# Performance work log

Hardware: AMD Instinct MI355X
Metric: run time of the kernel (lower is better)

## Reference

```python
import jax, jax.numpy as jnp
import numpy as np

D = 128  # feature = hidden = output dim (residuals force equality)


def setup_inputs() -> dict:
    key = jax.random.key(0)
    kx, k1, k2, kr = jax.random.split(key, 4)
    B, N = 8, 2048
    x = jax.random.normal(kx, (B, N, D), dtype=jnp.float32)
    w1 = jax.random.normal(k1, (D, D), dtype=jnp.float32)
    w2 = jax.random.normal(k2, (D, D), dtype=jnp.float32)
    wr = jax.random.normal(kr, (D, D), dtype=jnp.float32)
    return {"x": x, "w1": w1, "w2": w2, "wr": wr}


def reference(x, w1, w2, wr):
    # bilinear scores: [B, N, N]
    R = jnp.einsum('bnf,fg,bmg->bnm', x, wr, x)
    R = jax.nn.softmax(R, axis=2)
    # layer 1: relu(R @ x @ w1 + x)
    x = jax.nn.relu(jnp.einsum('bnm,bmf->bnf', R, x) @ w1 + x)
    # layer 2: relu(R @ x @ w2 + x)
    x = jax.nn.relu(jnp.einsum('bnm,bmf->bnf', R, x) @ w2 + x)
    return x[:, 0, :]
```

## Files before the change

kernel.cpp:

```cpp
#include <hip/hip_runtime.h>
#include <stdint.h>

typedef float  f32x4 __attribute__((ext_vector_type(4)));
typedef short  s16x8 __attribute__((ext_vector_type(8)));
typedef unsigned int u32;
typedef u32    u32x2 __attribute__((ext_vector_type(2)));
typedef u32    u32x4 __attribute__((ext_vector_type(4)));
typedef unsigned short u16;

#define MFMA16(a,b,c) __builtin_amdgcn_mfma_f32_16x16x32_bf16((a),(b),(c),0,0,0)

__device__ __forceinline__ u16 f2bf(float f){
  u32 u = __float_as_uint(f);
  return (u16)((u + 0x7fffu + ((u >> 16) & 1u)) >> 16);
}
__device__ __forceinline__ float bf2f(u16 h){ return __uint_as_float(((u32)h) << 16); }
__device__ __forceinline__ u32 pack2bf(float a, float b){ return (u32)f2bf(a) | ((u32)f2bf(b) << 16); }
__device__ __forceinline__ u32 packtrunc(float a, float b){
  return (__float_as_uint(a) >> 16) | (__float_as_uint(b) & 0xffff0000u);
}
__device__ __forceinline__ f32x4 f4zero(){ f32x4 z; z[0]=0.f; z[1]=0.f; z[2]=0.f; z[3]=0.f; return z; }
__device__ __forceinline__ s16x8 mk8(u32 a, u32 b, u32 c, u32 d){
  u32x4 w; w[0]=a; w[1]=b; w[2]=c; w[3]=d;
  return __builtin_bit_cast(s16x8, w);
}

__device__ __forceinline__ void async16(const void* g, void* l){
  __builtin_amdgcn_global_load_lds(
      (const __attribute__((address_space(1))) unsigned int*)g,
      (__attribute__((address_space(3))) unsigned int*)l, 16, 0, 0);
}

__global__ __launch_bounds__(256) void k_prep(
    const float* __restrict__ x, const float* __restrict__ wr, const float* __restrict__ w1,
    u16* __restrict__ xh, u16* __restrict__ xl, u16* __restrict__ Xt,
    u16* __restrict__ w1t, u16* __restrict__ yh, u16* __restrict__ yl)
{
  __shared__ __align__(16) char smem[65536];
  const int tid = threadIdx.x, bid = blockIdx.x;

  if (bid < 1024){
    float (*xs)[132] = (float(*)[132])smem;
    const long base = (long)bid * 2048;
#pragma unroll
    for (int k = 0; k < 8; k++){
      int idx = tid + k*256;
      float v = x[base + idx];
      xs[idx>>7][idx&127] = v;
      u16 h = f2bf(v);
      xh[base+idx] = h;
      xl[base+idx] = f2bf(v - bf2f(h));
    }
    __syncthreads();
    const int b  = bid >> 7;
    const int n0 = (bid & 127) * 16;
    const int nn = tid & 15, d0 = tid >> 4;
#pragma unroll
    for (int d = 0; d < 8; d++){
      int dd = d0 + d*16;
      Xt[(long)b*262144 + (long)dd*2048 + n0 + nn] = f2bf(xs[nn][dd]);
    }
  } else if (bid < 1032){
    const int base = (bid - 1024) * 2048;
#pragma unroll
    for (int k = 0; k < 8; k++){
      int idx = base + k*256 + tid;
      int c = idx >> 7, f = idx & 127;
      w1t[idx] = f2bf(w1[f*128 + c]);
    }
  } else {
    u16* sbh = (u16*)smem;
    u16* sbl = sbh + 16384;
    {
      const int c = tid & 127, f0 = (tid >> 7) * 64;
      const int key = (c & 7) << 4;
#pragma unroll
      for (int fi = 0; fi < 64; fi += 2){
        int f = f0 + fi;
        float v0 = wr[f*128 + c], v1 = wr[(f+1)*128 + c];
        u16 h0 = f2bf(v0), h1 = f2bf(v1);
        u32 hw = (u32)h0 | ((u32)h1 << 16);
        u32 lw = (u32)f2bf(v0 - bf2f(h0)) | ((u32)f2bf(v1 - bf2f(h1)) << 16);
        int byte = c*256 + ((((2*f) & ~15) ^ key) + ((2*f) & 15));
        *(u32*)((char*)sbh + byte) = hw;
        *(u32*)((char*)sbl + byte) = lw;
      }
    }
    __syncthreads();
    const int w = tid >> 6, lane = tid & 63, lr = lane & 15, g = lane >> 4;
    const long rowbase = (long)(bid - 1032)*128 + w*32;
    s16x8 ah[2][4], al[2][4];
#pragma unroll
    for (int rh = 0; rh < 2; rh++)
#pragma unroll
      for (int kc = 0; kc < 4; kc++){
        long r = rowbase + rh*16 + lr;
        const float4* px = (const float4*)(x + r*128 + kc*32 + g*8);
        float4 a = px[0], bV = px[1];
        u32 hh0, hh1, hh2, hh3, ll0, ll1, ll2, ll3;
        { u16 p=f2bf(a.x), q=f2bf(a.y); hh0=(u32)p|((u32)q<<16);
          ll0=(u32)f2bf(a.x-bf2f(p))|((u32)f2bf(a.y-bf2f(q))<<16); }
        { u16 p=f2bf(a.z), q=f2bf(a.w); hh1=(u32)p|((u32)q<<16);
          ll1=(u32)f2bf(a.z-bf2f(p))|((u32)f2bf(a.w-bf2f(q))<<16); }
        { u16 p=f2bf(bV.x), q=f2bf(bV.y); hh2=(u32)p|((u32)q<<16);
          ll2=(u32)f2bf(bV.x-bf2f(p))|((u32)f2bf(bV.y-bf2f(q))<<16); }
        { u16 p=f2bf(bV.z), q=f2bf(bV.w); hh3=(u32)p|((u32)q<<16);
          ll3=(u32)f2bf(bV.z-bf2f(p))|((u32)f2bf(bV.w-bf2f(q))<<16); }
        ah[rh][kc] = mk8(hh0,hh1,hh2,hh3);
        al[rh][kc] = mk8(ll0,ll1,ll2,ll3);
      }
    f32x4 acc[2][8];
#pragma unroll
    for (int rh = 0; rh < 2; rh++)
#pragma unroll
      for (int cg = 0; cg < 8; cg++) acc[rh][cg] = f4zero();
    const int swz = (lr & 7) << 4;
#pragma unroll
    for (int cg = 0; cg < 8; cg++){
      const int rowt = (cg*16 + lr) * 256;
#pragma unroll
      for (int kc = 0; kc < 4; kc++){
        int boff = rowt + ((kc*64 + g*16) ^ swz);
        s16x8 bh = *(const s16x8*)((const char*)sbh + boff);
        s16x8 bl = *(const s16x8*)((const char*)sbl + boff);
#pragma unroll
        for (int rh = 0; rh < 2; rh++){
          acc[rh][cg] = MFMA16(ah[rh][kc], bh, acc[rh][cg]);
          acc[rh][cg] = MFMA16(al[rh][kc], bh, acc[rh][cg]);
          acc[rh][cg] = MFMA16(ah[rh][kc], bl, acc[rh][cg]);
        }
      }
    }
#pragma unroll
    for (int rh = 0; rh < 2; rh++)
#pragma unroll
      for (int cg = 0; cg < 8; cg++)
#pragma unroll
        for (int r = 0; r < 4; r++){
          long q = rowbase + rh*16 + 4*g + r;
          int  c = cg*16 + lr;
          float v = acc[rh][cg][r] * 1.4426950408889634f;
          u16 h = f2bf(v);
          yh[q*128 + c] = h;
          yl[q*128 + c] = f2bf(v - bf2f(h));
        }
  }
}

__global__ __launch_bounds__(512) void k_flash(
    const u16* __restrict__ xh, const u16* __restrict__ xl, const u16* __restrict__ Xt,
    const u16* __restrict__ yh, const u16* __restrict__ yl,
    u16* __restrict__ Opart, float* __restrict__ mpart, float* __restrict__ lpart,
    float* __restrict__ S0, int KS, int kslog)
{
  __shared__ __align__(16) char lds[49152];
  const int tid = threadIdx.x, bid = blockIdx.x;
  const int b     = bid & 7;
  const int inner = bid >> 3;
  const int s     = inner & (KS - 1);
  const int qbl   = inner >> kslog;
  const int qb    = b*16 + qbl;
  const int nspan = 2048 >> kslog;
  const int kv0   = s * nspan;
  const int ntiles = nspan >> 5;
  const int w = tid >> 6, lane = tid & 63, lr = lane & 15, g = lane >> 4;
  const long qrow = (long)qb*128 + w*16;

  const int soff = w*1024 + lane*16;
  const int sswo = soff ^ (((soff >> 8) & 7) << 4);
  const int trow = soff >> 6;
  const int tsrc = trow*4096 + ((soff & 63) ^ ((trow & 3) << 4));
  const int bS0 = lr*256 + (( 0 + g*16) ^ ((lr & 7) << 4));
  const int bS1 = lr*256 + (( 64 + g*16) ^ ((lr & 7) << 4));
  const int bS2 = lr*256 + ((128 + g*16) ^ ((lr & 7) << 4));
  const int bS3 = lr*256 + ((192 + g*16) ^ ((lr & 7) << 4));
  const int bPV = lr*64 + ((g*16) ^ ((lr & 3) << 4));

  s16x8 byh[4], byl[4];
#pragma unroll
  for (int kc = 0; kc < 4; kc++){
    long r = qrow + lr;
    byh[kc] = *(const s16x8*)(yh + r*128 + kc*32 + g*8);
    byl[kc] = *(const s16x8*)(yl + r*128 + kc*32 + g*8);
  }

  f32x4 o[8];
#pragma unroll
  for (int dg = 0; dg < 8; dg++) o[dg] = f4zero();
  float mrun = -1e30f, lrun = 0.f;

  const char* gxh  = (const char*)xh + ((long)b*2048 + kv0)*256;
  const char* gxl  = (const char*)xl + ((long)b*2048 + kv0)*256;
  const char* gxtb = (const char*)(Xt + (long)b*262144 + kv0);

  auto stage = [&](int bufi, int t){
    char* dst = lds + bufi*8192 + w*1024;
    async16(gxh  + (long)t*8192 + sswo, dst);
    async16(gxl  + (long)t*8192 + sswo, dst + 16384);
    async16(gxtb + (long)t*64   + tsrc, dst + 32768);
  };

  stage(0, 0);
  __syncthreads();

  for (int t = 0; t < ntiles; t++){
    const int cur = t & 1;
    const char* pb = lds + cur*8192;
    const char* a0 = pb + bS0;
    const char* a1 = pb + bS1;
    const char* a2 = pb + bS2;
    const char* a3 = pb + bS3;

    f32x4 sacc[2];
    sacc[0] = f4zero(); sacc[1] = f4zero();
    __builtin_amdgcn_s_setprio(1);
#pragma unroll
    for (int ch = 0; ch < 2; ch++){
      const int co = ch*4096;
      s16x8 fh, fl;
      fh = *(const s16x8*)(a0 + co); fl = *(const s16x8*)(a0 + 16384 + co);
      sacc[ch] = MFMA16(fh, byh[0], sacc[ch]);
      sacc[ch] = MFMA16(fl, byh[0], sacc[ch]);
      sacc[ch] = MFMA16(fh, byl[0], sacc[ch]);
      fh = *(const s16x8*)(a1 + co); fl = *(const s16x8*)(a1 + 16384 + co);
      sacc[ch] = MFMA16(fh, byh[1], sacc[ch]);
      sacc[ch] = MFMA16(fl, byh[1], sacc[ch]);
      sacc[ch] = MFMA16(fh, byl[1], sacc[ch]);
      fh = *(const s16x8*)(a2 + co); fl = *(const s16x8*)(a2 + 16384 + co);
      sacc[ch] = MFMA16(fh, byh[2], sacc[ch]);
      sacc[ch] = MFMA16(fl, byh[2], sacc[ch]);
      sacc[ch] = MFMA16(fh, byl[2], sacc[ch]);
      fh = *(const s16x8*)(a3 + co); fl = *(const s16x8*)(a3 + 16384 + co);
      sacc[ch] = MFMA16(fh, byh[3], sacc[ch]);
      sacc[ch] = MFMA16(fl, byh[3], sacc[ch]);
      sacc[ch] = MFMA16(fh, byl[3], sacc[ch]);
    }
    __builtin_amdgcn_s_setprio(0);

    if (t + 1 < ntiles) stage(cur ^ 1, t + 1);

    if (qbl == 0 && w == 0 && lr == 0){
      float* s0p = S0 + b*2048 + kv0 + t*32 + 4*g;
#pragma unroll
      for (int ch = 0; ch < 2; ch++)
#pragma unroll
        for (int r = 0; r < 4; r++)
          s0p[ch*16 + r] = sacc[ch][r];
    }

    float cm = fmaxf(fmaxf(fmaxf(sacc[0][0], sacc[0][1]),
                           fmaxf(sacc[0][2], sacc[0][3])),
                     fmaxf(fmaxf(sacc[1][0], sacc[1][1]),
                           fmaxf(sacc[1][2], sacc[1][3])));
    cm = fmaxf(cm, __shfl_xor(cm, 16, 64));
    cm = fmaxf(cm, __shfl_xor(cm, 32, 64));
    if (__any(cm > mrun + 8.f)){
      float mn = fmaxf(mrun, cm);
      float sc = exp2f(mrun - mn);
#pragma unroll
      for (int dg = 0; dg < 8; dg++)
#pragma unroll
        for (int r = 0; r < 4; r++) o[dg][r] *= sc;
      lrun *= sc;
      mrun = mn;
    }
    float p[2][4];
#pragma unroll
    for (int ch = 0; ch < 2; ch++)
#pragma unroll
      for (int r = 0; r < 4; r++) p[ch][r] = exp2f(sacc[ch][r] - mrun);
    float ls = ((p[0][0] + p[0][1]) + (p[0][2] + p[0][3]))
             + ((p[1][0] + p[1][1]) + (p[1][2] + p[1][3]));
    ls += __shfl_xor(ls, 16, 64);
    ls += __shfl_xor(ls, 32, 64);
    lrun += ls;
    s16x8 bpq;
    {
      u32 pw00 = packtrunc(p[0][0], p[0][1]);
      u32 pw01 = packtrunc(p[0][2], p[0][3]);
      u32 pw10 = packtrunc(p[1][0], p[1][1]);
      u32 pw11 = packtrunc(p[1][2], p[1][3]);
      int sA = ((g & 1) << 5) + lr;
      int sB = sA + 16;
      u32 a0s = (u32)__shfl((int)pw00, sA, 64);
      u32 a1s = (u32)__shfl((int)pw01, sA, 64);
      u32 a2s = (u32)__shfl((int)pw10, sA, 64);
      u32 a3s = (u32)__shfl((int)pw11, sA, 64);
      u32 b0s = (u32)__shfl((int)pw00, sB, 64);
      u32 b1s = (u32)__shfl((int)pw01, sB, 64);
      u32 b2s = (u32)__shfl((int)pw10, sB, 64);
      u32 b3s = (u32)__shfl((int)pw11, sB, 64);
      bool hi = (g >= 2);
      bpq = mk8(hi ? a2s : a0s, hi ? a3s : a1s, hi ? b2s : b0s, hi ? b3s : b1s);
    }

    const char* ap = pb + 32768 + bPV;
    __builtin_amdgcn_s_setprio(1);
#pragma unroll
    for (int half = 0; half < 2; half++){
      s16x8 ax[4];
#pragma unroll
      for (int i = 0; i < 4; i++)
        ax[i] = *(const s16x8*)(ap + (half*4 + i)*1024);
#pragma unroll
      for (int i = 0; i < 4; i++)
        o[half*4 + i] = MFMA16(ax[i], bpq, o[half*4 + i]);
    }
    __builtin_amdgcn_s_setprio(0);
    __syncthreads();
  }

  {
    int lq = w*16 + lr;
    long bi = (long)(qbl*8 + b)*128 + lq;
    u16* op = Opart + bi*(long)(128 << kslog) + s*128;
#pragma unroll
    for (int dg = 0; dg < 8; dg++){
      u32x2 pw;
      pw[0] = pack2bf(o[dg][0], o[dg][1]);
      pw[1] = pack2bf(o[dg][2], o[dg][3]);
      *(u32x2*)(op + dg*16 + 4*g) = pw;
    }
    if (g == 0){
      mpart[bi*KS + s] = mrun;
      lpart[bi*KS + s] = lrun;
    }
  }
}

__global__ __launch_bounds__(256) void k_mergeL1(
    const u16* __restrict__ Opart, const float* __restrict__ mpart, const float* __restrict__ lpart,
    const u16* __restrict__ w1t, const float* __restrict__ x,
    const float* __restrict__ S0,
    float* __restrict__ A2p, float* __restrict__ Lj, float* __restrict__ x1r0,
    int KS)
{
  __shared__ u16 sb[16384];
  __shared__ u16 sa[4096];
  __shared__ float eS[32];
  __shared__ float redw[4][64];
  const int tid = threadIdx.x, bid = blockIdx.x;
  const int bb   = bid >> 6;
  const int qbl  = (bid >> 2) & 15;
  const int rb   = (bid & 3) * 32;
  const long R0  = (long)bid*32;
#pragma unroll
  for (int k = 0; k < 8; k++){
    int off = (tid + k*256)*16;
    int row = off >> 8;
    *(s16x8*)((char*)sb + (off ^ ((row & 7) << 4))) = *(const s16x8*)((const char*)w1t + off);
  }
  if (tid < 32){
    const float* mp0 = mpart + (long)(bb*128)*KS;
    float M = -1e30f;
    for (int s = 0; s < KS; s++) M = fmaxf(M, mp0[s]);
    eS[tid] = exp2f(S0[bb*2048 + (bid & 63)*32 + tid] - M);
  }
#pragma unroll
  for (int k = 0; k < 2; k++){
    int gidx = tid + k*256;
    int lrow = gidx >> 4, gcol = gidx & 15;
    long bi = (long)(qbl*8 + bb)*128 + rb + lrow;
    const float* mp = mpart + bi*KS;
    const float* lp = lpart + bi*KS;
    float m = -1e30f;
    for (int s = 0; s < KS; s++) m = fmaxf(m, mp[s]);
    float ls = 0.f;
    float a0=0.f,a1=0.f,a2=0.f,a3=0.f,a4=0.f,a5=0.f,a6=0.f,a7=0.f;
    const u16* ob = Opart + bi*(long)(KS*128) + gcol*8;
    for (int s = 0; s < KS; s++){
      float wgt = exp2f(mp[s] - m);
      ls += lp[s] * wgt;
      u32x4 v = *(const u32x4*)(ob + s*128);
      a0 += bf2f((u16)(v[0] & 0xffff)) * wgt;  a1 += bf2f((u16)(v[0] >> 16)) * wgt;
      a2 += bf2f((u16)(v[1] & 0xffff)) * wgt;  a3 += bf2f((u16)(v[1] >> 16)) * wgt;
      a4 += bf2f((u16)(v[2] & 0xffff)) * wgt;  a5 += bf2f((u16)(v[2] >> 16)) * wgt;
      a6 += bf2f((u16)(v[3] & 0xffff)) * wgt;  a7 += bf2f((u16)(v[3] >> 16)) * wgt;
    }
    float inv = 1.f / ls;
    u32x4 pw;
    pw[0] = pack2bf(a0*inv, a1*inv); pw[1] = pack2bf(a2*inv, a3*inv);
    pw[2] = pack2bf(a4*inv, a5*inv); pw[3] = pack2bf(a6*inv, a7*inv);
    int off = lrow*256 + gcol*16;
    *(u32x4*)((char*)sa + (off ^ ((lrow & 7) << 4))) = pw;
  }
  __syncthreads();
  const int w = tid >> 6, lane = tid & 63, lr = lane & 15, g = lane >> 4;
  const int rowhalf = w & 1, colhalf = w >> 1;
  s16x8 aa[4];
#pragma unroll
  for (int kc = 0; kc < 4; kc++){
    int lrow = rowhalf*16 + lr;
    aa[kc] = *(const s16x8*)((const char*)sa +
               (lrow*256 + ((kc*64 + g*16) ^ ((lrow & 7) << 4))));
  }
  f32x4 acc[4];
#pragma unroll
  for (int cg = 0; cg < 4; cg++) acc[cg] = f4zero();
  const int swz = (lr & 7) << 4;
#pragma unroll
  for (int cg = 0; cg < 4; cg++){
    const int c = colhalf*64 + cg*16 + lr;
    const int rowt = c*256;
#pragma unroll
    for (int kc = 0; kc < 4; kc++){
      s16x8 bV = *(const s16x8*)((const char*)sb + rowt + ((kc*64 + g*16) ^ swz));
      acc[cg] = MFMA16(aa[kc], bV, acc[cg]);
    }
  }
  const float e0 = eS[rowhalf*16 + 4*g + 0];
  const float e1 = eS[rowhalf*16 + 4*g + 1];
  const float e2 = eS[rowhalf*16 + 4*g + 2];
  const float e3 = eS[rowhalf*16 + 4*g + 3];
  float sA2[4];
#pragma unroll
  for (int cg = 0; cg < 4; cg++){
    int c = colhalf*64 + cg*16 + lr;
    f32x4 vv;
#pragma unroll
    for (int r = 0; r < 4; r++){
      long q = R0 + rowhalf*16 + 4*g + r;
      vv[r] = fmaxf(acc[cg][r] + x[q*128 + c], 0.f);
    }
    if (((bid & 63) == 0) && rowhalf == 0 && g == 0)
      x1r0[bb*128 + c] = vv[0];
    sA2[cg] = e0*vv[0] + e1*vv[1] + e2*vv[2] + e3*vv[3];
  }
#pragma unroll
  for (int cg = 0; cg < 4; cg++){
    sA2[cg] += __shfl_xor(sA2[cg], 16, 64);
    sA2[cg] += __shfl_xor(sA2[cg], 32, 64);
  }
  if (g == 0){
#pragma unroll
    for (int cg = 0; cg < 4; cg++) redw[w][cg*16 + lr] = sA2[cg];
  }
  __syncthreads();
  if (tid < 128){
    int cl = tid & 63, pair = (tid >> 6) * 2;
    A2p[(long)bid*128 + tid] = redw[pair][cl] + redw[pair + 1][cl];
  }
  if (w == 2){
    float v = (lane < 32) ? eS[lane] : 0.f;
    v += __shfl_xor(v, 1, 64);  v += __shfl_xor(v, 2, 64);
    v += __shfl_xor(v, 4, 64);  v += __shfl_xor(v, 8, 64);
    v += __shfl_xor(v, 16, 64); v += __shfl_xor(v, 32, 64);
    if (lane == 0) Lj[bid] = v;
  }
}

__global__ __launch_bounds__(256) void k_out(
    const float* __restrict__ A2p, const float* __restrict__ Lj,
    const float* __restrict__ w2, const float* __restrict__ x1r0,
    float* __restrict__ out)
{
  __shared__ float a2s[2][128];
  const int tid = threadIdx.x, bid = blockIdx.x;
  const int b0 = bid*2;
  {
    int which = tid >> 7, f = tid & 127;
    int bb = b0 + which;
    float s = 0.f, L = 0.f;
#pragma unroll
    for (int jj = 0; jj < 64; jj++){
      s += A2p[(long)(bb*64 + jj)*128 + f];
      L += Lj[bb*64 + jj];
    }
    a2s[which][f] = s / L;
  }
  __syncthreads();
  const int which = tid >> 7, d = tid & 127;
  const int b = b0 + which;
  float acc = x1r0[b*128 + d];
  for (int f = 0; f < 128; f++)
    acc += a2s[which][f] * w2[f*128 + d];
  out[b*128 + d] = fmaxf(acc, 0.f);
}

extern "C" void kernel_launch(void* const* d_in, const int* in_sizes, int n_in,
                              void* d_out, int out_size, void* d_ws, size_t ws_size,
                              hipStream_t stream)
{
  const float* x  = (const float*)d_in[0];
  const float* w1 = (const float*)d_in[1];
  const float* w2 = (const float*)d_in[2];
  const float* wr = (const float*)d_in[3];
  float* out = (float*)d_out;
  char* ws = (char*)d_ws;

  u16*   xh      = (u16*)  (ws + 0);
  u16*   xl      = (u16*)  (ws + 4194304);
  u16*   Xt      = (u16*)  (ws + 8388608);
  u16*   yh      = (u16*)  (ws + 12582912);
  u16*   yl      = (u16*)  (ws + 16777216);
  u16*   w1t     = (u16*)  (ws + 20971520);
  float* S0      = (float*)(ws + 21004288);
  float* Lj      = (float*)(ws + 21070848);
  float* A2p     = (float*)(ws + 21072896);
  float* x1r0    = (float*)(ws + 21335040);
  const size_t tail = 21339136;

  int KS = 4, kslog = 2;
  while (KS > 1 && tail + (size_t)KS*4325376ull > ws_size){ KS >>= 1; kslog--; }
  float* mpart = (float*)(ws + tail);
  float* lpart = (float*)(ws + tail + (size_t)KS*65536);
  u16*   Opart = (u16*)  (ws + tail + (size_t)KS*131072);

  k_prep   <<<1160, 256, 0, stream>>>(x, wr, w1, xh, xl, Xt, w1t, yh, yl);
  k_flash  <<<128*KS, 512, 0, stream>>>(xh, xl, Xt, yh, yl, Opart, mpart, lpart, S0, KS, kslog);
  k_mergeL1<<<512, 256, 0, stream>>>(Opart, mpart, lpart, w1t, x, S0, A2p, Lj, x1r0, KS);
  k_out    <<<4, 256, 0, stream>>>(A2p, Lj, w2, x1r0, out);
}
```

Before: 82.38 us.

## Fuse x split/transpose into y-projection blocks and parallelize output kernel per batch

The prep kernel no longer runs separate blocks that split x into bf16 hi/lo and transpose it. Each projection block now handles 64 rows, reuses the x hi/lo fragments it already built for the MFMA, stages them in swizzled LDS and writes xh, xl and the transposed Xt with vectorized 16-byte stores. This removes a second read of x and the scalar 2-byte transposed stores, at the cost of fewer, heavier blocks (264 instead of 1160). The output kernel now uses one block per batch, splits the reductions across both thread halves and sums L with a warp shuffle, which raises parallelism in that tail kernel.

```diff
diff --git a/kernel.cpp b/kernel.cpp
--- a/kernel.cpp
+++ b/kernel.cpp
@@ -39,111 +39,123 @@
   __shared__ __align__(16) char smem[65536];
   const int tid = threadIdx.x, bid = blockIdx.x;
 
-  if (bid < 1024){
-    float (*xs)[132] = (float(*)[132])smem;
-    const long base = (long)bid * 2048;
-#pragma unroll
-    for (int k = 0; k < 8; k++){
-      int idx = tid + k*256;
-      float v = x[base + idx];
-      xs[idx>>7][idx&127] = v;
-      u16 h = f2bf(v);
-      xh[base+idx] = h;
-      xl[base+idx] = f2bf(v - bf2f(h));
-    }
-    __syncthreads();
-    const int b  = bid >> 7;
-    const int n0 = (bid & 127) * 16;
-    const int nn = tid & 15, d0 = tid >> 4;
-#pragma unroll
-    for (int d = 0; d < 8; d++){
-      int dd = d0 + d*16;
-      Xt[(long)b*262144 + (long)dd*2048 + n0 + nn] = f2bf(xs[nn][dd]);
-    }
-  } else if (bid < 1032){
-    const int base = (bid - 1024) * 2048;
+  if (bid < 8){
+    const int base = bid * 2048;
 #pragma unroll
     for (int k = 0; k < 8; k++){
       int idx = base + k*256 + tid;
       int c = idx >> 7, f = idx & 127;
       w1t[idx] = f2bf(w1[f*128 + c]);
     }
-  } else {
-    u16* sbh = (u16*)smem;
-    u16* sbl = sbh + 16384;
-    {
-      const int c = tid & 127, f0 = (tid >> 7) * 64;
-      const int key = (c & 7) << 4;
-#pragma unroll
-      for (int fi = 0; fi < 64; fi += 2){
-        int f = f0 + fi;
-        float v0 = wr[f*128 + c], v1 = wr[(f+1)*128 + c];
-        u16 h0 = f2bf(v0), h1 = f2bf(v1);
-        u32 hw = (u32)h0 | ((u32)h1 << 16);
-        u32 lw = (u32)f2bf(v0 - bf2f(h0)) | ((u32)f2bf(v1 - bf2f(h1)) << 16);
-        int byte = c*256 + ((((2*f) & ~15) ^ key) + ((2*f) & 15));
-        *(u32*)((char*)sbh + byte) = hw;
-        *(u32*)((char*)sbl + byte) = lw;
-      }
-    }
-    __syncthreads();
-    const int w = tid >> 6, lane = tid & 63, lr = lane & 15, g = lane >> 4;
-    const long rowbase = (long)(bid - 1032)*128 + w*32;
-    s16x8 ah[2][4], al[2][4];
-#pragma unroll
-    for (int rh = 0; rh < 2; rh++)
-#pragma unroll
-      for (int kc = 0; kc < 4; kc++){
-        long r = rowbase + rh*16 + lr;
-        const float4* px = (const float4*)(x + r*128 + kc*32 + g*8);
-        float4 a = px[0], bV = px[1];
-        u32 hh0, hh1, hh2, hh3, ll0, ll1, ll2, ll3;
-        { u16 p=f2bf(a.x), q=f2bf(a.y); hh0=(u32)p|((u32)q<<16);
-          ll0=(u32)f2bf(a.x-bf2f(p))|((u32)f2bf(a.y-bf2f(q))<<16); }
-        { u16 p=f2bf(a.z), q=f2bf(a.w); hh1=(u32)p|((u32)q<<16);
-          ll1=(u32)f2bf(a.z-bf2f(p))|((u32)f2bf(a.w-bf2f(q))<<16); }
-        { u16 p=f2bf(bV.x), q=f2bf(bV.y); hh2=(u32)p|((u32)q<<16);
-          ll2=(u32)f2bf(bV.x-bf2f(p))|((u32)f2bf(bV.y-bf2f(q))<<16); }
-        { u16 p=f2bf(bV.z), q=f2bf(bV.w); hh3=(u32)p|((u32)q<<16);
-          ll3=(u32)f2bf(bV.z-bf2f(p))|((u32)f2bf(bV.w-bf2f(q))<<16); }
-        ah[rh][kc] = mk8(hh0,hh1,hh2,hh3);
-        al[rh][kc] = mk8(ll0,ll1,ll2,ll3);
-      }
-    f32x4 acc[2][8];
-#pragma unroll
-    for (int rh = 0; rh < 2; rh++)
-#pragma unroll
-      for (int cg = 0; cg < 8; cg++) acc[rh][cg] = f4zero();
-    const int swz = (lr & 7) << 4;
-#pragma unroll
-    for (int cg = 0; cg < 8; cg++){
-      const int rowt = (cg*16 + lr) * 256;
-#pragma unroll
-      for (int kc = 0; kc < 4; kc++){
-        int boff = rowt + ((kc*64 + g*16) ^ swz);
-        s16x8 bh = *(const s16x8*)((const char*)sbh + boff);
-        s16x8 bl = *(const s16x8*)((const char*)sbl + boff);
-#pragma unroll
-        for (int rh = 0; rh < 2; rh++){
-          acc[rh][cg] = MFMA16(ah[rh][kc], bh, acc[rh][cg]);
-          acc[rh][cg] = MFMA16(al[rh][kc], bh, acc[rh][cg]);
-          acc[rh][cg] = MFMA16(ah[rh][kc], bl, acc[rh][cg]);
-        }
-      }
-    }
-#pragma unroll
-    for (int rh = 0; rh < 2; rh++)
-#pragma unroll
-      for (int cg = 0; cg < 8; cg++)
-#pragma unroll
-        for (int r = 0; r < 4; r++){
-          long q = rowbase + rh*16 + 4*g + r;
-          int  c = cg*16 + lr;
-          float v = acc[rh][cg][r] * 1.4426950408889634f;
-          u16 h = f2bf(v);
-          yh[q*128 + c] = h;
-          yl[q*128 + c] = f2bf(v - bf2f(h));
-        }
+    return;
+  }
+  u16* sbh = (u16*)smem;
+  u16* sbl = sbh + 16384;
+  {
+    const int c = tid & 127, f0 = (tid >> 7) * 64;
+    const int key = (c & 7) << 4;
+#pragma unroll
+    for (int fi = 0; fi < 64; fi += 2){
+      int f = f0 + fi;
+      float v0 = wr[f*128 + c], v1 = wr[(f+1)*128 + c];
+      u16 h0 = f2bf(v0), h1 = f2bf(v1);
+      u32 hw = (u32)h0 | ((u32)h1 << 16);
+      u32 lw = (u32)f2bf(v0 - bf2f(h0)) | ((u32)f2bf(v1 - bf2f(h1)) << 16);
+      int byte = c*256 + ((((2*f) & ~15) ^ key) + ((2*f) & 15));
+      *(u32*)((char*)sbh + byte) = hw;
+      *(u32*)((char*)sbl + byte) = lw;
+    }
+  }
+  __syncthreads();
+  const int w = tid >> 6, lane = tid & 63, lr = lane & 15, g = lane >> 4;
+  const int bidp = bid - 8;
+  const long rowbase = (long)bidp * 64;
+  s16x8 ah[4], al[4];
+#pragma unroll
+  for (int kc = 0; kc < 4; kc++){
+    long r = rowbase + w*16 + lr;
+    const float4* px = (const float4*)(x + r*128 + kc*32 + g*8);
+    float4 a = px[0], bV = px[1];
+    u32 hh0, hh1, hh2, hh3, ll0, ll1, ll2, ll3;
+    { u16 p=f2bf(a.x), q=f2bf(a.y); hh0=(u32)p|((u32)q<<16);
+      ll0=(u32)f2bf(a.x-bf2f(p))|((u32)f2bf(a.y-bf2f(q))<<16); }
+    { u16 p=f2bf(a.z), q=f2bf(a.w); hh1=(u32)p|((u32)q<<16);
+      ll1=(u32)f2bf(a.z-bf2f(p))|((u32)f2bf(a.w-bf2f(q))<<16); }
+    { u16 p=f2bf(bV.x), q=f2bf(bV.y); hh2=(u32)p|((u32)q<<16);
+      ll2=(u32)f2bf(bV.x-bf2f(p))|((u32)f2bf(bV.y-bf2f(q))<<16); }
+    { u16 p=f2bf(bV.z), q=f2bf(bV.w); hh3=(u32)p|((u32)q<<16);
+      ll3=(u32)f2bf(bV.z-bf2f(p))|((u32)f2bf(bV.w-bf2f(q))<<16); }
+    ah[kc] = mk8(hh0,hh1,hh2,hh3);
+    al[kc] = mk8(ll0,ll1,ll2,ll3);
+  }
+  f32x4 acc[8];
+#pragma unroll
+  for (int cg = 0; cg < 8; cg++) acc[cg] = f4zero();
+  const int swz = (lr & 7) << 4;
+#pragma unroll
+  for (int cg = 0; cg < 8; cg++){
+    const int rowt = (cg*16 + lr) * 256;
+#pragma unroll
+    for (int kc = 0; kc < 4; kc++){
+      int boff = rowt + ((kc*64 + g*16) ^ swz);
+      s16x8 bh = *(const s16x8*)((const char*)sbh + boff);
+      s16x8 bl = *(const s16x8*)((const char*)sbl + boff);
+      acc[cg] = MFMA16(ah[kc], bh, acc[cg]);
+      acc[cg] = MFMA16(al[kc], bh, acc[cg]);
+      acc[cg] = MFMA16(ah[kc], bl, acc[cg]);
+    }
+  }
+#pragma unroll
+  for (int cg = 0; cg < 8; cg++)
+#pragma unroll
+    for (int r = 0; r < 4; r++){
+      long q = rowbase + w*16 + 4*g + r;
+      int  c = cg*16 + lr;
+      float v = acc[cg][r] * 1.4426950408889634f;
+      u16 h = f2bf(v);
+      yh[q*128 + c] = h;
+      yl[q*128 + c] = f2bf(v - bf2f(h));
+    }
+  __syncthreads();
+#pragma unroll
+  for (int kc = 0; kc < 4; kc++){
+    int off = (w*16 + lr)*256 + ((kc*64 + g*16) ^ swz);
+    *(s16x8*)(smem + off)         = ah[kc];
+    *(s16x8*)(smem + 16384 + off) = al[kc];
+  }
+  __syncthreads();
+  {
+    char* gbh = (char*)xh + rowbase*256;
+    char* gbl = (char*)xl + rowbase*256;
+#pragma unroll
+    for (int it = 0; it < 4; it++){
+      int off = (tid + it*256)*16;
+      int row = off >> 8;
+      int so = off ^ ((row & 7) << 4);
+      *(s16x8*)(gbh + off) = *(const s16x8*)(smem + so);
+      *(s16x8*)(gbl + off) = *(const s16x8*)(smem + 16384 + so);
+    }
+  }
+  {
+    const int b  = bidp >> 5;
+    const int n0 = (bidp & 31) * 64;
+    const int d  = tid >> 1, nh = tid & 1;
+    u16 tmp[32];
+#pragma unroll
+    for (int j = 0; j < 32; j++){
+      int n = nh*32 + j;
+      int byte = n*256 + ((((d >> 3) << 4) ^ ((n & 7) << 4))) + (d & 7)*2;
+      tmp[j] = *(const u16*)(smem + byte);
+    }
+    u16* dst = Xt + (long)b*262144 + (long)d*2048 + n0 + nh*32;
+#pragma unroll
+    for (int j2 = 0; j2 < 4; j2++){
+      s16x8 v = mk8((u32)tmp[j2*8+0] | ((u32)tmp[j2*8+1] << 16),
+                    (u32)tmp[j2*8+2] | ((u32)tmp[j2*8+3] << 16),
+                    (u32)tmp[j2*8+4] | ((u32)tmp[j2*8+5] << 16),
+                    (u32)tmp[j2*8+6] | ((u32)tmp[j2*8+7] << 16));
+      *(s16x8*)(dst + j2*8) = v;
+    }
   }
 }
 
@@ -454,27 +466,33 @@
     const float* __restrict__ w2, const float* __restrict__ x1r0,
     float* __restrict__ out)
 {
-  __shared__ float a2s[2][128];
-  const int tid = threadIdx.x, bid = blockIdx.x;
-  const int b0 = bid*2;
-  {
-    int which = tid >> 7, f = tid & 127;
-    int bb = b0 + which;
-    float s = 0.f, L = 0.f;
-#pragma unroll
-    for (int jj = 0; jj < 64; jj++){
-      s += A2p[(long)(bb*64 + jj)*128 + f];
-      L += Lj[bb*64 + jj];
-    }
-    a2s[which][f] = s / L;
-  }
-  __syncthreads();
-  const int which = tid >> 7, d = tid & 127;
-  const int b = b0 + which;
-  float acc = x1r0[b*128 + d];
-  for (int f = 0; f < 128; f++)
-    acc += a2s[which][f] * w2[f*128 + d];
-  out[b*128 + d] = fmaxf(acc, 0.f);
+  __shared__ float a2s[128];
+  __shared__ float partial[128];
+  __shared__ float Lsh;
+  const int tid = threadIdx.x, b = blockIdx.x;
+  const int f = tid & 127, h = tid >> 7;
+  float s = 0.f;
+  for (int jj = h*32; jj < h*32 + 32; jj++)
+    s += A2p[(long)(b*64 + jj)*128 + f];
+  if (h == 1) partial[f] = s;
+  if (tid < 64){
+    float Lp = Lj[b*64 + tid];
+    Lp += __shfl_xor(Lp, 1, 64);  Lp += __shfl_xor(Lp, 2, 64);
+    Lp += __shfl_xor(Lp, 4, 64);  Lp += __shfl_xor(Lp, 8, 64);
+    Lp += __shfl_xor(Lp, 16, 64); Lp += __shfl_xor(Lp, 32, 64);
+    if (tid == 0) Lsh = Lp;
+  }
+  __syncthreads();
+  if (h == 0) a2s[f] = (s + partial[f]) / Lsh;
+  __syncthreads();
+  const int d = tid & 127, fh = tid >> 7;
+  float acc = 0.f;
+  for (int f2 = fh*64; f2 < fh*64 + 64; f2++)
+    acc += a2s[f2] * w2[f2*128 + d];
+  if (fh == 1) partial[d] = acc;
+  __syncthreads();
+  if (fh == 0)
+    out[b*128 + d] = fmaxf(acc + partial[d] + x1r0[b*128 + d], 0.f);
 }
 
 extern "C" void kernel_launch(void* const* d_in, const int* in_sizes, int n_in,
@@ -506,8 +524,8 @@
   float* lpart = (float*)(ws + tail + (size_t)KS*65536);
   u16*   Opart = (u16*)  (ws + tail + (size_t)KS*131072);
 
-  k_prep   <<<1160, 256, 0, stream>>>(x, wr, w1, xh, xl, Xt, w1t, yh, yl);
+  k_prep   <<<264, 256, 0, stream>>>(x, wr, w1, xh, xl, Xt, w1t, yh, yl);
   k_flash  <<<128*KS, 512, 0, stream>>>(xh, xl, Xt, yh, yl, Opart, mpart, lpart, S0, KS, kslog);
   k_mergeL1<<<512, 256, 0, stream>>>(Opart, mpart, lpart, w1t, x, S0, A2p, Lj, x1r0, KS);
-  k_out    <<<4, 256, 0, stream>>>(A2p, Lj, w2, x1r0, out);
-}
+  k_out    <<<8, 256, 0, stream>>>(A2p, Lj, w2, x1r0, out);
+}
```

New measurement: 76.75 us. -6.8%, faster.
